# Performance work log

Hardware: AMD Instinct MI355X
Metric: run time of the kernel (lower is better)

## Reference

```python
import jax, jax.numpy as jnp
import numpy as np
from jax import lax

B, C_IN, T_FRAMES = 64, 128, 200
AUDIO_LEN = 48000
N_BANDS = 32


def _filter_shapes():
    lin = np.linspace(0.0, 1.0, N_BANDS, dtype=np.float32)
    fs = np.stack([
        np.exp(-0.5 * ((lin - 0.2) / 0.1) ** 2),
        np.exp(-0.5 * ((lin - 0.1) / 0.1) ** 2),
        np.exp(-0.5 * ((lin - 0.4) / 0.15) ** 2),
        np.exp(-0.5 * ((lin - 0.6) / 0.1) ** 2),
        np.linspace(0.1, 1.0, N_BANDS, dtype=np.float32) ** 2,
    ]).astype(np.float32)
    return fs


def _linear_interp(x, out_len):
    # PyTorch F.interpolate(mode='linear', align_corners=False) along last dim
    t_in = x.shape[-1]
    src = (jnp.arange(out_len, dtype=jnp.float32) + 0.5) * (t_in / out_len) - 0.5
    src = jnp.clip(src, 0.0, float(t_in - 1))
    i0 = jnp.floor(src).astype(jnp.int32)
    i1 = jnp.minimum(i0 + 1, t_in - 1)
    w = (src - i0).astype(x.dtype)
    return x[..., i0] * (1.0 - w) + x[..., i1] * w


def _conv1d(x, w, b, pad):
    y = lax.conv_general_dilated(x, w, (1,), [(pad, pad)],
                                 dimension_numbers=('NCH', 'OIH', 'NCH'))
    return y + b[None, :, None]


def _band_index(num_bins):
    # bin k belongs to band b iff int(b*num_bins/32) <= k < int((b+1)*num_bins/32)
    bounds = np.array([int(b * num_bins / N_BANDS) for b in range(N_BANDS + 1)])
    idx = np.searchsorted(bounds, np.arange(num_bins), side='right') - 1
    return np.clip(idx, 0, N_BANDS - 1)


def _forward(condition, f0, white_noise, w1, b1, w2, b2, w3, b3, w4, b4, audio_length):
    leaky = lambda v: jnp.where(v >= 0, v, 0.1 * v)
    is_voiced = (f0 > 0).astype(condition.dtype)[:, None, :]                 # [B,1,T]
    x = jnp.concatenate([condition, is_voiced], axis=1)                       # [B,129,T]
    h = leaky(_conv1d(x, w1, b1, 2))
    h = leaky(_conv1d(h, w2, b2, 1))
    h = leaky(_conv1d(h, w3, b3, 1))
    p = _conv1d(h, w4, b4, 0)                                                 # [B,40,T]
    inhal = jax.nn.sigmoid(p[:, 0:1])
    exhal = jax.nn.sigmoid(p[:, 1:2])
    pressure = jax.nn.sigmoid(p[:, 2:3])
    spectral_shape = jax.nn.softmax(p[:, 3:35], axis=1)                       # [B,32,T]
    turbulence = jax.nn.softmax(p[:, 35:40], axis=1)                          # [B,5,T]
    breath_features = jnp.concatenate([pressure, inhal, exhal], axis=1)       # [B,3,T]
    control = jnp.concatenate([inhal, exhal, pressure, turbulence], axis=1)   # [B,8,T]
    # --- FFT colored noise shaping (single block since L <= 60000) ---
    num_bins = audio_length // 2 + 1
    avg_shape = jnp.mean(spectral_shape, axis=2)                              # [B,32]
    gains = avg_shape[:, _band_index(num_bins)]                               # [B,bins]
    nfft = jnp.fft.rfft(white_noise[:, 0, :])                                 # [B,bins]
    shaped = jnp.fft.irfft(nfft * gains, n=audio_length)                      # [B,L]
    shaped = shaped / jnp.std(shaped, axis=1, ddof=1, keepdims=True) * 0.1
    breath_noise = shaped[:, None, :]                                         # [B,1,L]
    # --- linear upsample frame-rate controls to audio rate ---
    ctrl_a = _linear_interp(control, audio_length)                            # [B,8,L]
    voiced_a = _linear_interp(is_voiced, audio_length)                        # [B,1,L]
    inh_a, exh_a, pr_a = ctrl_a[:, 0:1], ctrl_a[:, 1:2], ctrl_a[:, 2:3]
    turb_a = ctrl_a[:, 3:8]                                                   # [B,5,L]
    breath = breath_noise * inh_a * (1.0 - voiced_a) + breath_noise * exh_a * pr_a
    # --- turbulence-location spectral filtering (vectorized over 5 locs) ---
    bfft = jnp.fft.rfft(breath[:, 0, :])                                      # [B,bins]
    fbins = _linear_interp(jnp.asarray(_filter_shapes())[None], num_bins)[0]  # [5,bins]
    loc_w = jnp.mean(turb_a, axis=2)                                          # [B,5]
    total_filter = loc_w @ fbins                                              # [B,bins]
    filtered = jnp.fft.irfft(bfft * total_filter, n=audio_length)[:, None, :]
    return filtered, breath_features


def setup_inputs() -> dict:
    key = jax.random.key(0)
    ks = jax.random.split(key, 7)
    s = 0.05
    return {
        'condition': jax.random.normal(ks[0], (B, C_IN, T_FRAMES), jnp.float32),
        'f0': jax.random.normal(ks[1], (B, T_FRAMES), jnp.float32),
        'white_noise': jax.random.normal(ks[2], (B, 1, AUDIO_LEN), jnp.float32),
        'w1': jax.random.normal(ks[3], (256, C_IN + 1, 5), jnp.float32) * s,
        'b1': jnp.zeros((256,), jnp.float32),
        'w2': jax.random.normal(ks[4], (128, 256, 3), jnp.float32) * s,
        'b2': jnp.zeros((128,), jnp.float32),
        'w3': jax.random.normal(ks[5], (64, 128, 3), jnp.float32) * s,
        'b3': jnp.zeros((64,), jnp.float32),
        'w4': jax.random.normal(ks[6], (40, 64, 1), jnp.float32) * s,
        'b4': jnp.zeros((40,), jnp.float32),
        'audio_length': AUDIO_LEN,
    }


def reference(condition, f0, white_noise, w1, b1, w2, b2, w3, b3, w4, b4, audio_length):
    return _forward(condition, f0, white_noise, w1, b1, w2, b2, w3, b3, w4, b4, audio_length)
```

## Files before the change

### kernel.cpp

```cpp
#include <hip/hip_runtime.h>
#include <math.h>

#define BB 64
#define T_FR 200
#define NA 48000
#define NBINS 24001

typedef __attribute__((ext_vector_type(4))) float f32x4;
typedef __attribute__((ext_vector_type(8))) short bf16x8;

__device__ __forceinline__ unsigned short f2bf(float x)
{
    unsigned u = __float_as_uint(x);
    u = (u + 0x7FFFu + ((u >> 16) & 1u)) >> 16;
    return (unsigned short)u;
}
__device__ __forceinline__ float bf2f(unsigned short h)
{
    return __uint_as_float(((unsigned)h) << 16);
}

__device__ __forceinline__ float2 cmul(float2 a, float2 b)
{
    return make_float2(a.x * b.x - a.y * b.y, a.x * b.y + a.y * b.x);
}
__device__ __forceinline__ float2 cadd(float2 a, float2 b){ return make_float2(a.x+b.x, a.y+b.y); }
__device__ __forceinline__ float2 csub(float2 a, float2 b){ return make_float2(a.x-b.x, a.y-b.y); }

__device__ __forceinline__ float2 cis_rev(float rev)
{
    return make_float2(__builtin_amdgcn_cosf(rev), __builtin_amdgcn_sinf(rev));
}

template<int R> __device__ __forceinline__ void fill_roots(float (&cr)[R], float (&si)[R]);
template<> __device__ __forceinline__ void fill_roots<3>(float (&cr)[3], float (&si)[3])
{
    const float S = 0.86602540378443865f;
    cr[0]=1.f; cr[1]=-0.5f; cr[2]=-0.5f;
    si[0]=0.f; si[1]=S;     si[2]=-S;
}
template<> __device__ __forceinline__ void fill_roots<5>(float (&cr)[5], float (&si)[5])
{
    cr[0]=1.f; cr[1]=0.30901699437494742f; cr[2]=-0.80901699437494742f;
    cr[3]=-0.80901699437494742f; cr[4]=0.30901699437494742f;
    si[0]=0.f; si[1]=0.95105651629515357f; si[2]=0.58778525229247313f;
    si[3]=-0.58778525229247313f; si[4]=-0.95105651629515357f;
}
template<> __device__ __forceinline__ void fill_roots<8>(float (&cr)[8], float (&si)[8])
{
    const float C = 0.70710678118654752f;
    cr[0]=1.f; cr[1]=C;  cr[2]=0.f;  cr[3]=-C; cr[4]=-1.f; cr[5]=-C;  cr[6]=0.f;  cr[7]=C;
    si[0]=0.f; si[1]=C;  si[2]=1.f;  si[3]=C;  si[4]=0.f;  si[5]=-C;  si[6]=-1.f; si[7]=-C;
}

template<int S, int R>
__device__ __forceinline__ void dftR(float2 (&v)[R])
{
    float cr[R], si[R];
    fill_roots<R>(cr, si);
    float2 o[R];
#pragma unroll
    for (int k = 0; k < R; ++k) {
        float re = 0.f, im = 0.f;
#pragma unroll
        for (int j = 0; j < R; ++j) {
            int m = (j * k) % R;
            float ur = cr[m], ui = (S > 0) ? si[m] : -si[m];
            re += v[j].x * ur - v[j].y * ui;
            im += v[j].x * ui + v[j].y * ur;
        }
        o[k] = make_float2(re, im);
    }
#pragma unroll
    for (int k = 0; k < R; ++k) v[k] = o[k];
}

__device__ __constant__ float C25R[17] = {1.f,0.968583161f,0.876306680f,0.728968627f,0.535826795f,0.309016994f,0.062790520f,-0.187381315f,-0.425779292f,-0.637423990f,-0.809016994f,-0.929776486f,-0.992114701f,-0.992114701f,-0.929776486f,-0.809016994f,-0.637423990f};
__device__ __constant__ float C25I[17] = {0.f,0.248689887f,0.481753674f,0.684547106f,0.844327926f,0.951056516f,0.998026728f,0.982287251f,0.904827052f,0.770513243f,0.587785252f,0.368124553f,0.125333234f,-0.125333234f,-0.368124553f,-0.587785252f,-0.770513243f};
__device__ __constant__ float C15R[9] = {1.f,0.913545458f,0.669130606f,0.309016994f,-0.104528463f,-0.5f,-0.809016994f,-0.978147601f,-0.978147601f};
__device__ __constant__ float C15I[9] = {0.f,0.406736643f,0.743144825f,0.951056516f,0.994521895f,0.866025404f,0.587785252f,0.207911691f,-0.207911691f};
__device__ __constant__ float C16R[10] = {1.f,0.923879533f,0.707106781f,0.382683432f,0.f,-0.382683432f,-0.707106781f,-0.923879533f,-1.f,-0.923879533f};
__device__ __constant__ float C16I[10] = {0.f,0.382683432f,0.707106781f,0.923879533f,1.f,0.923879533f,0.707106781f,0.382683432f,0.f,-0.382683432f};

template<int S> __device__ __forceinline__ float2 tw25(int m){ return make_float2(C25R[m], S>0? C25I[m] : -C25I[m]); }
template<int S> __device__ __forceinline__ float2 tw15(int m){ return make_float2(C15R[m], S>0? C15I[m] : -C15I[m]); }
template<int S> __device__ __forceinline__ float2 tw16(int m){ return make_float2(C16R[m], S>0? C16I[m] : -C16I[m]); }

template<int S> __device__ __forceinline__ void f4(float2& x0, float2& x1, float2& x2, float2& x3)
{
    float2 e = cadd(x0,x2), f = csub(x0,x2), g = cadd(x1,x3), h = csub(x1,x3);
    float2 r = (S<0) ? make_float2(h.y, -h.x) : make_float2(-h.y, h.x);
    x0 = cadd(e,g); x2 = csub(e,g); x1 = cadd(f,r); x3 = csub(f,r);
}

template<int S> __device__ __forceinline__ void fft16(float2 (&v)[16])
{
    float2 t[4][4];
#pragma unroll
    for (int q = 0; q < 4; ++q) {
        float2 a = v[q], b = v[4+q], c = v[8+q], d = v[12+q];
        f4<S>(a,b,c,d);
        t[q][0]=a; t[q][1]=b; t[q][2]=c; t[q][3]=d;
    }
#pragma unroll
    for (int q = 1; q < 4; ++q)
#pragma unroll
        for (int r = 1; r < 4; ++r)
            t[q][r] = cmul(t[q][r], tw16<S>(q*r));
#pragma unroll
    for (int r = 0; r < 4; ++r) {
        float2 a=t[0][r], b=t[1][r], c=t[2][r], d=t[3][r];
        f4<S>(a,b,c,d);
        v[r]=a; v[r+4]=b; v[r+8]=c; v[r+12]=d;
    }
}

template<int S> __device__ __forceinline__ void fft15(float2 (&v)[15])
{
    float2 t[5][3];
#pragma unroll
    for (int d = 0; d < 5; ++d) {
        float2 u[3] = { v[d], v[5+d], v[10+d] };
        dftR<S,3>(u);
        t[d][0]=u[0];
        t[d][1]=cmul(u[1], tw15<S>(d));
        t[d][2]=cmul(u[2], tw15<S>(2*d));
    }
#pragma unroll
    for (int e = 0; e < 3; ++e) {
        float2 u[5] = { t[0][e],t[1][e],t[2][e],t[3][e],t[4][e] };
        dftR<S,5>(u);
#pragma unroll
        for (int g = 0; g < 5; ++g) v[e + 3*g] = u[g];
    }
}

template<int S> __device__ __forceinline__ void fft25(float2 (&v)[25])
{
    float2 t[5][5];
#pragma unroll
    for (int d = 0; d < 5; ++d) {
        float2 u[5] = { v[d], v[5+d], v[10+d], v[15+d], v[20+d] };
        dftR<S,5>(u);
        t[d][0] = u[0];
#pragma unroll
        for (int e = 1; e < 5; ++e) t[d][e] = cmul(u[e], tw25<S>(d*e));
    }
#pragma unroll
    for (int e = 0; e < 5; ++e) {
        float2 u[5] = { t[0][e],t[1][e],t[2][e],t[3][e],t[4][e] };
        dftR<S,5>(u);
#pragma unroll
        for (int g = 0; g < 5; ++g) v[e + 5*g] = u[g];
    }
}

__device__ __forceinline__ int slotn(int f) { return 25 * (f & 7) + (f >> 3); }

__device__ __forceinline__ void pair_combine(float2 Za, float2 Zb, float g1, float g2,
                                             float2& C, float2& Cp, float& e1, float& e2)
{
    float2 X1 = make_float2(0.5f * (Za.x + Zb.x), 0.5f * (Za.y - Zb.y));
    float2 w  = make_float2(0.5f * (Za.x - Zb.x), 0.5f * (Za.y + Zb.y));
    float2 X2 = make_float2(w.y, -w.x);
    float2 Z1 = make_float2(g1 * X1.x, g1 * X1.y);
    float2 Z2 = make_float2(g2 * X2.x, g2 * X2.y);
    e1 = Z1.x * Z1.x + Z1.y * Z1.y;
    e2 = Z2.x * Z2.x + Z2.y * Z2.y;
    C  = make_float2(Z1.x - Z2.y,  Z1.y + Z2.x);
    Cp = make_float2(Z1.x + Z2.y, -Z1.y + Z2.x);
}

template<int NT, int TAPS, int CHUNKS, int CINP, int COUTP>
__global__ __launch_bounds__(256) void conv_mfma_kernel(
    const unsigned short* __restrict__ xT, int tRowsIn,
    const unsigned short* __restrict__ wT,
    const float* __restrict__ bias,
    unsigned short* __restrict__ outT, int tRowsOut, int tOffOut)
{
    const int b = blockIdx.y;
    const int t0 = blockIdx.x * 16;
    const int tid = threadIdx.x;
    const int wave = tid >> 6;
    const int lane = tid & 63;
    const int m = lane & 15;
    const int quad = lane >> 4;
    const int n0 = wave * (NT * 16);

    f32x4 acc[NT];
#pragma unroll
    for (int nt = 0; nt < NT; ++nt) acc[nt] = (f32x4){0.f, 0.f, 0.f, 0.f};

    const unsigned short* xb = xT + (size_t)b * tRowsIn * CINP;
#pragma unroll
    for (int kw = 0; kw < TAPS; ++kw) {
        const unsigned short* wk = wT + (size_t)kw * COUTP * CINP;
        const unsigned short* xrow = xb + (size_t)(t0 + kw + m) * CINP + quad * 8;
#pragma unroll
        for (int ch = 0; ch < CHUNKS; ++ch) {
            const int k0 = ch * 32;
            bf16x8 a = *(const bf16x8*)(xrow + k0);
#pragma unroll
            for (int nt = 0; nt < NT; ++nt) {
                bf16x8 bfr = *(const bf16x8*)(wk + (size_t)(n0 + nt * 16 + m) * CINP + k0 + quad * 8);
                acc[nt] = __builtin_amdgcn_mfma_f32_16x16x32_bf16(a, bfr, acc[nt], 0, 0, 0);
            }
        }
    }
#pragma unroll
    for (int nt = 0; nt < NT; ++nt) {
        const int n = n0 + nt * 16 + m;
        const float bz = bias[n];
#pragma unroll
        for (int r = 0; r < 4; ++r) {
            const int t = t0 + quad * 4 + r;
            if (t < 200) {
                float v = acc[nt][r] + bz;
                v = (v >= 0.f) ? v : 0.1f * v;
                outT[((size_t)b * tRowsOut + t + tOffOut) * COUTP + n] = f2bf(v);
            }
        }
    }
}

__global__ void prep_x1_kernel(const float* __restrict__ cond, const float* __restrict__ f0,
                               unsigned short* __restrict__ xpT1)
{
    int idx = blockIdx.x * 256 + threadIdx.x;
    const int total = BB * 212 * 160;
    if (idx >= total) return;
    int i = idx % 160;
    int rest = idx / 160;
    int tp = rest % 212;
    int b = rest / 212;
    int tt = tp - 2;
    float v = 0.f;
    if (tt >= 0 && tt < 200) {
        if (i < 128) v = cond[((size_t)b * 128 + i) * 200 + tt];
        else if (i == 128) v = (f0[b * 200 + tt] > 0.f) ? 1.f : 0.f;
    }
    xpT1[idx] = f2bf(v);
}

template<int TAPS, int CINR, int CINP, int COUTP>
__global__ void prep_w_kernel(const float* __restrict__ w, unsigned short* __restrict__ wT)
{
    int idx = blockIdx.x * 256 + threadIdx.x;
    const int total = TAPS * COUTP * CINP;
    if (idx >= total) return;
    int i = idx % CINP;
    int rest = idx / CINP;
    int o = rest % COUTP;
    int kw = rest / COUTP;
    float v = (i < CINR) ? w[((size_t)o * CINR + i) * TAPS + kw] : 0.f;
    wT[idx] = f2bf(v);
}

__global__ void zero16_kernel(uint4* __restrict__ p, int n16)
{
    int idx = blockIdx.x * 256 + threadIdx.x;
    if (idx < n16) p[idx] = make_uint4(0, 0, 0, 0);
}


__global__ __launch_bounds__(128) void passA_kernel(const float* __restrict__ wn,
                                                    float2* __restrict__ I)
{
    __shared__ float2 L[8 * 241];
    int q = blockIdx.y;
    const float* w1p = wn + (size_t)(2 * q) * NA;
    const float* w2p = wn + (size_t)(2 * q + 1) * NA;
    int n20 = blockIdx.x * 8;
    int tid = threadIdx.x;

    if (tid < 120) {
        int b = tid >> 3, j = tid & 7;
        int n2 = n20 + j;
        float2 v[16];
#pragma unroll
        for (int a = 0; a < 16; ++a) {
            int n = (15 * a + b) * 200 + n2;
            v[a] = make_float2(w1p[n], w2p[n]);
        }
        fft16<-1>(v);
#pragma unroll
        for (int f1 = 1; f1 < 16; ++f1)
            v[f1] = cmul(v[f1], cis_rev(-(float)(b * f1) * (1.f / 240.f)));
        float2* col = L + j * 241;
#pragma unroll
        for (int f1 = 0; f1 < 16; ++f1) col[f1 * 15 + b] = v[f1];
    }
    __syncthreads();
    {
        int f1 = tid >> 3, j = tid & 7;
        int n2 = n20 + j;
        float2* col = L + j * 241;
        float2 u[15];
#pragma unroll
        for (int b = 0; b < 15; ++b) u[b] = col[f1 * 15 + b];
        fft15<-1>(u);
#pragma unroll
        for (int f2 = 0; f2 < 15; ++f2) {
            int f = f1 + 16 * f2;
            I[(size_t)q * NA + (size_t)f * 200 + n2] =
                cmul(u[f2], cis_rev(-(float)(n2 * f) * (1.f / (float)NA)));
        }
    }
}

template<int MODE>
__global__ __launch_bounds__(256) void passB_kernel(float2* __restrict__ I,
    const float* __restrict__ avg_shape, const float* __restrict__ fbins,
    const float* __restrict__ loc_w, float* __restrict__ acc, float* __restrict__ z0)
{
    __shared__ float2 L[12 * 202];
    __shared__ float g1sh[32], g2sh[32];
    int q = blockIdx.y;
    int b1 = 2 * q, b2 = 2 * q + 1;
    int bx = blockIdx.x;
    int tid = threadIdx.x;
    if (MODE == 0) {
        if (tid < 32) { g1sh[tid] = avg_shape[b1 * 32 + tid]; g2sh[tid] = avg_shape[b2 * 32 + tid]; }
    } else {
        if (tid < 5) { g1sh[tid] = loc_w[b1 * 5 + tid]; g2sh[tid] = loc_w[b2 * 5 + tid]; }
    }
    int Rrow[12];
#pragma unroll
    for (int s = 0; s < 12; ++s) {
        int p = s >> 1;
        int pi = 6 * bx + p;
        Rrow[s] = (pi == 0) ? ((s & 1) ? 120 : 0) : ((s & 1) ? 240 - pi : pi);
    }
    for (int idx = tid; idx < 300; idx += 256) {
        int s = idx / 25, b = idx - 25 * s;
        const float2* g = I + (size_t)q * NA + (size_t)Rrow[s] * 200;
        float2 v[8];
#pragma unroll
        for (int a = 0; a < 8; ++a) v[a] = g[25 * a + b];
        dftR<-1, 8>(v);
#pragma unroll
        for (int f1 = 1; f1 < 8; ++f1)
            v[f1] = cmul(v[f1], cis_rev(-(float)(b * f1) * (1.f / 200.f)));
        float2* row = L + s * 202;
#pragma unroll
        for (int f1 = 0; f1 < 8; ++f1) row[f1 * 25 + b] = v[f1];
    }
    __syncthreads();
    if (tid < 96) {
        int s = tid >> 3, f1 = tid & 7;
        float2* row = L + s * 202;
        float2 u[25];
#pragma unroll
        for (int b = 0; b < 25; ++b) u[b] = row[f1 * 25 + b];
        fft25<-1>(u);
#pragma unroll
        for (int f2 = 0; f2 < 25; ++f2) row[f1 * 25 + f2] = u[f2];
    }
    __syncthreads();
    float part1 = 0.f, part2 = 0.f;
    for (int idx = tid; idx < 1206; idx += 256) {
        int p = idx / 201, t = idx - p * 201;
        int pi = 6 * bx + p;
        float2* rwA = L + (2 * p) * 202;
        float2* rwB = L + (2 * p + 1) * 202;
        int k = -1;
        float2 Za, Zb;
        int sa = 0, sb = 0;
        float2* wa = rwA; float2* wb = rwB;
        bool self1 = false;
        if (pi != 0) {
            if (t >= 200) continue;
            sa = slotn(t); sb = slotn(199 - t);
            Za = rwA[sa]; Zb = rwB[sb];
            k = pi + 240 * t;
        } else if (t < 101) {
            wa = rwA; wb = rwA;
            if (t == 0 || t == 100) {
                sa = slotn(t); sb = sa;
                Za = rwA[sa]; Zb = Za;
                k = 240 * t;
                self1 = true;
            } else {
                sa = slotn(t); sb = slotn(200 - t);
                Za = rwA[sa]; Zb = rwA[sb];
                k = 240 * t;
            }
        } else {
            int t2 = t - 101;
            if (t2 >= 100) continue;
            wa = rwB; wb = rwB;
            sa = slotn(t2); sb = slotn(199 - t2);
            Za = rwB[sa]; Zb = rwB[sb];
            k = 120 + 240 * t2;
        }
        int kbin = min(k, NA - k);
        float g1, g2;
        if (MODE == 0) {
            int jj = (kbin * 32) / NBINS;
            if (jj < 31 && (NBINS * (jj + 1)) / 32 <= kbin) ++jj;
            g1 = g1sh[jj]; g2 = g2sh[jj];
        } else {
            g1 = 0.f; g2 = 0.f;
#pragma unroll
            for (int c = 0; c < 5; ++c) {
                float fb = fbins[c * NBINS + kbin];
                g1 += g1sh[c] * fb; g2 += g2sh[c] * fb;
            }
        }
        float2 C, Cp; float e1, e2;
        pair_combine(Za, Zb, g1, g2, C, Cp, e1, e2);
        if (MODE == 0) {
            float wgt = self1 ? 1.f : 2.f;
            part1 += wgt * e1; part2 += wgt * e2;
            if (k == 0) { z0[b1] = g1 * Za.x; z0[b2] = g2 * Za.y; }
        }
        wa[sa] = make_float2(C.x * (1.f / NA), C.y * (1.f / NA));
        if (!self1) wb[sb] = make_float2(Cp.x * (1.f / NA), Cp.y * (1.f / NA));
    }
    if (MODE == 0) {
        for (int o = 32; o > 0; o >>= 1) {
            part1 += __shfl_down(part1, o);
            part2 += __shfl_down(part2, o);
        }
        if ((tid & 63) == 0) { atomicAdd(&acc[b1], part1); atomicAdd(&acc[b2], part2); }
    }
    __syncthreads();
    if (tid < 96) {
        int s = tid >> 3, f1 = tid & 7;
        float2* row = L + s * 202;
        float2 u[25];
#pragma unroll
        for (int f2 = 0; f2 < 25; ++f2) u[f2] = row[f1 * 25 + f2];
        fft25<+1>(u);
#pragma unroll
        for (int b = 0; b < 25; ++b) row[f1 * 25 + b] = u[b];
    }
    __syncthreads();
    for (int idx = tid; idx < 300; idx += 256) {
        int s = idx / 25, b = idx - 25 * s;
        float2* row = L + s * 202;
        float2 w[8];
#pragma unroll
        for (int f1 = 0; f1 < 8; ++f1) w[f1] = row[f1 * 25 + b];
#pragma unroll
        for (int f1 = 1; f1 < 8; ++f1)
            w[f1] = cmul(w[f1], cis_rev((float)(b * f1) * (1.f / 200.f)));
        dftR<+1, 8>(w);
        int rg = Rrow[s];
        float2* g = I + (size_t)q * NA + (size_t)rg * 200;
#pragma unroll
        for (int a = 0; a < 8; ++a) {
            int e = 25 * a + b;
            g[e] = cmul(w[a], cis_rev((float)(e * rg) * (1.f / (float)NA)));
        }
    }
}

__global__ __launch_bounds__(128) void passC_kernel(float2* __restrict__ I,
    const float* __restrict__ control, const float* __restrict__ f0,
    const float* __restrict__ scale)
{
    __shared__ float2 L[8 * 241];
    __shared__ float ctlA[600], ctlB[600];
    __shared__ float f0A[200], f0B[200];
    int q = blockIdx.y;
    int b1 = 2 * q, b2 = 2 * q + 1;
    int n20 = blockIdx.x * 8;
    int tid = threadIdx.x;
    for (int i = tid; i < 600; i += 128) {
        ctlA[i] = control[(size_t)b1 * 1600 + i];
        ctlB[i] = control[(size_t)b2 * 1600 + i];
    }
    for (int i = tid; i < 200; i += 128) {
        f0A[i] = f0[b1 * 200 + i];
        f0B[i] = f0[b2 * 200 + i];
    }
    {
        int f1 = tid >> 3, j = tid & 7;
        int n2 = n20 + j;
        float2 u[15];
#pragma unroll
        for (int f2 = 0; f2 < 15; ++f2)
            u[f2] = I[(size_t)q * NA + (size_t)(f1 + 16 * f2) * 200 + n2];
        fft15<+1>(u);
        float2* col = L + j * 241;
#pragma unroll
        for (int b = 0; b < 15; ++b) col[f1 * 15 + b] = u[b];
    }
    __syncthreads();
    if (tid < 120) {
        int b = tid >> 3, j = tid & 7;
        int n2 = n20 + j;
        float2* col = L + j * 241;
        float sc1 = scale[b1], sc2 = scale[b2];
        float2 w[16];
#pragma unroll
        for (int f1 = 0; f1 < 16; ++f1) w[f1] = col[f1 * 15 + b];
#pragma unroll
        for (int f1 = 1; f1 < 16; ++f1)
            w[f1] = cmul(w[f1], cis_rev((float)(b * f1) * (1.f / 240.f)));
        fft16<+1>(w);
#pragma unroll
        for (int a = 0; a < 16; ++a) {
            int n = 200 * (15 * a + b) + n2;
            float sf = ((float)n + 0.5f) * (1.f / 240.f) - 0.5f;
            sf = fminf(fmaxf(sf, 0.f), 199.f);
            int i0 = (int)sf;
            int i1 = min(i0 + 1, 199);
            float wt = sf - (float)i0, w0 = 1.f - wt;
            float inh = ctlA[i0] * w0 + ctlA[i1] * wt;
            float exh = ctlA[200 + i0] * w0 + ctlA[200 + i1] * wt;
            float pr  = ctlA[400 + i0] * w0 + ctlA[400 + i1] * wt;
            float vv  = (f0A[i0] > 0.f ? 1.f : 0.f) * w0 + (f0A[i1] > 0.f ? 1.f : 0.f) * wt;
            float m1 = inh * (1.f - vv) + exh * pr;
            inh = ctlB[i0] * w0 + ctlB[i1] * wt;
            exh = ctlB[200 + i0] * w0 + ctlB[200 + i1] * wt;
            pr  = ctlB[400 + i0] * w0 + ctlB[400 + i1] * wt;
            vv  = (f0B[i0] > 0.f ? 1.f : 0.f) * w0 + (f0B[i1] > 0.f ? 1.f : 0.f) * wt;
            float m2 = inh * (1.f - vv) + exh * pr;
            w[a] = make_float2(w[a].x * sc1 * m1, w[a].y * sc2 * m2);
        }
        fft16<-1>(w);
#pragma unroll
        for (int f1 = 1; f1 < 16; ++f1)
            w[f1] = cmul(w[f1], cis_rev(-(float)(b * f1) * (1.f / 240.f)));
#pragma unroll
        for (int f1 = 0; f1 < 16; ++f1) col[f1 * 15 + b] = w[f1];
    }
    __syncthreads();
    {
        int f1 = tid >> 3, j = tid & 7;
        int n2 = n20 + j;
        float2* col = L + j * 241;
        float2 u[15];
#pragma unroll
        for (int b = 0; b < 15; ++b) u[b] = col[f1 * 15 + b];
        fft15<-1>(u);
#pragma unroll
        for (int f2 = 0; f2 < 15; ++f2) {
            int f = f1 + 16 * f2;
            I[(size_t)q * NA + (size_t)f * 200 + n2] =
                cmul(u[f2], cis_rev(-(float)(n2 * f) * (1.f / (float)NA)));
        }
    }
}

__global__ __launch_bounds__(128) void passD_kernel(const float2* __restrict__ I,
                                                    float* __restrict__ out)
{
    __shared__ float2 L[8 * 241];
    int q = blockIdx.y;
    int b1 = 2 * q, b2 = 2 * q + 1;
    int n20 = blockIdx.x * 8;
    int tid = threadIdx.x;
    {
        int f1 = tid >> 3, j = tid & 7;
        int n2 = n20 + j;
        float2 u[15];
#pragma unroll
        for (int f2 = 0; f2 < 15; ++f2)
            u[f2] = I[(size_t)q * NA + (size_t)(f1 + 16 * f2) * 200 + n2];
        fft15<+1>(u);
        float2* col = L + j * 241;
#pragma unroll
        for (int b = 0; b < 15; ++b) col[f1 * 15 + b] = u[b];
    }
    __syncthreads();
    if (tid < 120) {
        int b = tid >> 3, j = tid & 7;
        int n2 = n20 + j;
        float2* col = L + j * 241;
        float2 w[16];
#pragma unroll
        for (int f1 = 0; f1 < 16; ++f1) w[f1] = col[f1 * 15 + b];
#pragma unroll
        for (int f1 = 1; f1 < 16; ++f1)
            w[f1] = cmul(w[f1], cis_rev((float)(b * f1) * (1.f / 240.f)));
        fft16<+1>(w);
#pragma unroll
        for (int a = 0; a < 16; ++a) {
            int n = 200 * (15 * a + b) + n2;
            out[(size_t)b1 * NA + n] = w[a].x;
            out[(size_t)b2 * NA + n] = w[a].y;
        }
    }
}

__global__ void init_kernel(float* __restrict__ acc, float* __restrict__ z0)
{
    int i = threadIdx.x;
    if (i < 64) { acc[i] = 0.f; z0[i] = 0.f; }
}

__global__ void finalize_scale(const float* __restrict__ acc, const float* __restrict__ z0,
                               float* __restrict__ scale)
{
    int b = threadIdx.x;
    if (b < 64) {
        float var = (acc[b] - z0[b] * z0[b]) / (48000.f * 47999.f);
        scale[b] = 0.1f / sqrtf(var);
    }
}

__global__ void head_kernel(const unsigned short* __restrict__ h3T, const float* __restrict__ w4,
                            const float* __restrict__ b4, float* __restrict__ control,
                            float* __restrict__ avg_shape, float* __restrict__ out_bf)
{
    __shared__ float w4s[40 * 64];
    __shared__ float b4s[40];
    __shared__ float sp[200 * 33];
    int b = blockIdx.x;
    for (int j = threadIdx.x; j < 40 * 64; j += 256) w4s[j] = w4[j];
    if (threadIdx.x < 40) b4s[threadIdx.x] = b4[threadIdx.x];
    __syncthreads();
    int t = threadIdx.x;
    if (t < 200) {
        float p[40];
#pragma unroll
        for (int o = 0; o < 40; ++o) p[o] = b4s[o];
        const unsigned short* hb = h3T + ((size_t)b * 200 + t) * 64;
        for (int i = 0; i < 64; ++i) {
            float h = bf2f(hb[i]);
#pragma unroll
            for (int o = 0; o < 40; ++o) p[o] += h * w4s[o * 64 + i];
        }
        float inh = 1.f / (1.f + expf(-p[0]));
        float exh = 1.f / (1.f + expf(-p[1]));
        float pr  = 1.f / (1.f + expf(-p[2]));
        float mx = p[3];
#pragma unroll
        for (int c = 1; c < 32; ++c) mx = fmaxf(mx, p[3 + c]);
        float e[32];
        float sum = 0.f;
#pragma unroll
        for (int c = 0; c < 32; ++c) { e[c] = expf(p[3 + c] - mx); sum += e[c]; }
        float inv = 1.f / sum;
#pragma unroll
        for (int c = 0; c < 32; ++c) sp[t * 33 + c] = e[c] * inv;
        float mx2 = p[35];
#pragma unroll
        for (int c = 1; c < 5; ++c) mx2 = fmaxf(mx2, p[35 + c]);
        float e2[5];
        float s2 = 0.f;
#pragma unroll
        for (int c = 0; c < 5; ++c) { e2[c] = expf(p[35 + c] - mx2); s2 += e2[c]; }
        float inv2 = 1.f / s2;
        float* ctl = control + (size_t)b * 8 * 200;
        ctl[0 * 200 + t] = inh;
        ctl[1 * 200 + t] = exh;
        ctl[2 * 200 + t] = pr;
#pragma unroll
        for (int c = 0; c < 5; ++c) ctl[(3 + c) * 200 + t] = e2[c] * inv2;
        float* bf = out_bf + (size_t)b * 3 * 200;
        bf[0 * 200 + t] = pr;
        bf[1 * 200 + t] = inh;
        bf[2 * 200 + t] = exh;
    }
    __syncthreads();
    if (t < 32) {
        float s = 0.f;
        for (int j = 0; j < 200; ++j) s += sp[j * 33 + t];
        avg_shape[b * 32 + t] = s * (1.f / 200.f);
    }
}

__global__ void locw_mean_kernel(const float* __restrict__ control, float* __restrict__ loc_w)
{
    int c = blockIdx.x, b = blockIdx.y;
    int tid = threadIdx.x;
    const float* src = control + ((size_t)b * 8 + 3 + c) * 200;
    float s = (tid < 200) ? src[tid] : 0.f;
    for (int o = 32; o > 0; o >>= 1) s += __shfl_down(s, o);
    __shared__ float red[4];
    if ((tid & 63) == 0) red[tid >> 6] = s;
    __syncthreads();
    if (tid == 0) loc_w[b * 5 + c] = (red[0] + red[1] + red[2] + red[3]) * (1.f / 200.f);
}

__device__ inline float filter_shape_val(int c, int i)
{
    float lin = (float)i * (1.f / 31.f);
    if (c == 0) { float z = (lin - 0.2f) * 10.f;          return expf(-0.5f * z * z); }
    if (c == 1) { float z = (lin - 0.1f) * 10.f;          return expf(-0.5f * z * z); }
    if (c == 2) { float z = (lin - 0.4f) * (1.f / 0.15f); return expf(-0.5f * z * z); }
    if (c == 3) { float z = (lin - 0.6f) * 10.f;          return expf(-0.5f * z * z); }
    float v = 0.1f + 0.9f * lin;
    return v * v;
}

__global__ void fbins_kernel(float* __restrict__ fbins)
{
    int k = blockIdx.x * 256 + threadIdx.x;
    if (k >= NBINS) return;
    float sf = (k + 0.5f) * (32.0f / 24001.0f) - 0.5f;
    sf = fminf(fmaxf(sf, 0.f), 31.f);
    int i0 = (int)sf;
    int i1 = min(i0 + 1, 31);
    float w = sf - (float)i0;
#pragma unroll
    for (int c = 0; c < 5; ++c)
        fbins[c * NBINS + k] = filter_shape_val(c, i0) * (1.f - w) + filter_shape_val(c, i1) * w;
}

extern "C" void kernel_launch(void* const* d_in, const int* in_sizes, int n_in,
                              void* d_out, int out_size, void* d_ws, size_t ws_size,
                              hipStream_t stream)
{
    const float* cond = (const float*)d_in[0];
    const float* f0   = (const float*)d_in[1];
    const float* wn   = (const float*)d_in[2];
    const float* w1   = (const float*)d_in[3];
    const float* b1   = (const float*)d_in[4];
    const float* w2   = (const float*)d_in[5];
    const float* b2   = (const float*)d_in[6];
    const float* w3   = (const float*)d_in[7];
    const float* b3   = (const float*)d_in[8];
    const float* w4   = (const float*)d_in[9];
    const float* b4   = (const float*)d_in[10];

    float* out = (float*)d_out;
    float* filtered = out;
    float* bf_out   = out + (size_t)BB * NA;

    char* ws = (char*)d_ws;
    size_t off = 0;
    float2* I = (float2*)(ws + off);            off += 24576000;
    unsigned short* xpT1 = (unsigned short*)(ws + off); off += (size_t)BB * 212 * 160 * 2;
    unsigned short* xpT2 = (unsigned short*)(ws + off); off += (size_t)BB * 210 * 256 * 2;
    unsigned short* xpT3 = (unsigned short*)(ws + off); off += (size_t)BB * 210 * 128 * 2;
    unsigned short* xpT4 = (unsigned short*)(ws + off); off += (size_t)BB * 200 * 64 * 2;
    unsigned short* wT1  = (unsigned short*)(ws + off); off += (size_t)5 * 256 * 160 * 2;
    unsigned short* wT2  = (unsigned short*)(ws + off); off += (size_t)3 * 128 * 256 * 2;
    unsigned short* wT3  = (unsigned short*)(ws + off); off += (size_t)3 * 64 * 128 * 2;
    float* control   = (float*)(ws + off);
    float* avg_shape = control + 102400;
    float* loc_w     = avg_shape + 2048;
    float* acc       = loc_w + 320;
    float* z0        = acc + 64;
    float* scale     = z0 + 64;
    float* fbins     = scale + 64;

    dim3 blk(256);

    init_kernel<<<1, 64, 0, stream>>>(acc, z0);

    {
        int n1 = BB * 212 * 160;
        prep_x1_kernel<<<dim3((n1 + 255) / 256), blk, 0, stream>>>(cond, f0, xpT1);
        int z2 = (BB * 210 * 256 * 2) / 16;
        zero16_kernel<<<dim3((z2 + 255) / 256), blk, 0, stream>>>((uint4*)xpT2, z2);
        int z3 = (BB * 210 * 128 * 2) / 16;
        zero16_kernel<<<dim3((z3 + 255) / 256), blk, 0, stream>>>((uint4*)xpT3, z3);
        prep_w_kernel<5, 129, 160, 256><<<dim3((5 * 256 * 160 + 255) / 256), blk, 0, stream>>>(w1, wT1);
        prep_w_kernel<3, 256, 256, 128><<<dim3((3 * 128 * 256 + 255) / 256), blk, 0, stream>>>(w2, wT2);
        prep_w_kernel<3, 128, 128, 64><<<dim3((3 * 64 * 128 + 255) / 256), blk, 0, stream>>>(w3, wT3);
    }

    conv_mfma_kernel<4, 5, 5, 160, 256><<<dim3(13, BB), blk, 0, stream>>>(
        xpT1, 212, wT1, b1, xpT2, 210, 1);
    conv_mfma_kernel<2, 3, 8, 256, 128><<<dim3(13, BB), blk, 0, stream>>>(
        xpT2, 210, wT2, b2, xpT3, 210, 1);
    conv_mfma_kernel<1, 3, 4, 128, 64><<<dim3(13, BB), blk, 0, stream>>>(
        xpT3, 210, wT3, b3, xpT4, 200, 0);

    head_kernel<<<dim3(BB), blk, 0, stream>>>(xpT4, w4, b4, control, avg_shape, bf_out);
    locw_mean_kernel<<<dim3(5, BB), blk, 0, stream>>>(control, loc_w);
    fbins_kernel<<<dim3((NBINS + 255) / 256), blk, 0, stream>>>(fbins);

    passA_kernel<<<dim3(25, 32), dim3(128), 0, stream>>>(wn, I);
    passB_kernel<0><<<dim3(20, 32), blk, 0, stream>>>(I, avg_shape, fbins, loc_w, acc, z0);
    finalize_scale<<<1, 64, 0, stream>>>(acc, z0, scale);
    passC_kernel<<<dim3(25, 32), dim3(128), 0, stream>>>(I, control, f0, scale);
    passB_kernel<1><<<dim3(20, 32), blk, 0, stream>>>(I, avg_shape, fbins, loc_w, acc, z0);
    passD_kernel<<<dim3(25, 32), dim3(128), 0, stream>>>(I, filtered);
}
```

Before: 367.6 us.

## Fuse forward fft25, spectral combine and inverse fft25 in registers per thread

For non-DC row pairs, each thread now loads one A row and its mirrored B row, runs the forward 25-point FFT, applies the filter/energy combine on the paired bins, and runs the inverse FFT, all in registers. This removes two shared-memory round trips and two barriers-worth of separate phases for most blocks. The special pi==0 pair keeps the old path, but only in block 0. The cost is more registers per thread (two 25-element complex arrays) and work spread over only 12 lanes per wave.

New measurement: 634.7 us. 1.73x slower.

```diff
diff --git a/kernel.cpp b/kernel.cpp
--- a/kernel.cpp
+++ b/kernel.cpp
@@ -169,6 +169,37 @@
     e2 = Z2.x * Z2.x + Z2.y * Z2.y;
     C  = make_float2(Z1.x - Z2.y,  Z1.y + Z2.x);
     Cp = make_float2(Z1.x + Z2.y, -Z1.y + Z2.x);
+}
+
+template<int MODE>
+__device__ __forceinline__ void comb_one(float2& A, float2& B, int k, float wgt, bool self1,
+                                         const float* __restrict__ g1sh, const float* __restrict__ g2sh,
+                                         const float* __restrict__ fbins,
+                                         float& part1, float& part2,
+                                         float* __restrict__ z0, int b1, int b2)
+{
+    int kbin = min(k, NA - k);
+    float g1, g2;
+    if (MODE == 0) {
+        int jj = (kbin * 32) / NBINS;
+        if (jj < 31 && (NBINS * (jj + 1)) / 32 <= kbin) ++jj;
+        g1 = g1sh[jj]; g2 = g2sh[jj];
+    } else {
+        g1 = 0.f; g2 = 0.f;
+#pragma unroll
+        for (int c = 0; c < 5; ++c) {
+            float fb = fbins[c * NBINS + kbin];
+            g1 += g1sh[c] * fb; g2 += g2sh[c] * fb;
+        }
+    }
+    float2 C, Cp; float e1, e2;
+    pair_combine(A, B, g1, g2, C, Cp, e1, e2);
+    if (MODE == 0) {
+        part1 += wgt * e1; part2 += wgt * e2;
+        if (k == 0) { z0[b1] = g1 * A.x; z0[b2] = g2 * A.y; }
+    }
+    A = make_float2(C.x * (1.f / NA), C.y * (1.f / NA));
+    if (!self1) B = make_float2(Cp.x * (1.f / NA), Cp.y * (1.f / NA));
 }
 
 template<int NT, int TAPS, int CHUNKS, int CINP, int COUTP>
@@ -346,76 +377,100 @@
         for (int f1 = 0; f1 < 8; ++f1) row[f1 * 25 + b] = v[f1];
     }
     __syncthreads();
-    if (tid < 96) {
-        int s = tid >> 3, f1 = tid & 7;
-        float2* row = L + s * 202;
-        float2 u[25];
-#pragma unroll
-        for (int b = 0; b < 25; ++b) u[b] = row[f1 * 25 + b];
-        fft25<-1>(u);
-#pragma unroll
-        for (int f2 = 0; f2 < 25; ++f2) row[f1 * 25 + f2] = u[f2];
-    }
-    __syncthreads();
     float part1 = 0.f, part2 = 0.f;
-    for (int idx = tid; idx < 1206; idx += 256) {
-        int p = idx / 201, t = idx - p * 201;
-        int pi = 6 * bx + p;
-        float2* rwA = L + (2 * p) * 202;
-        float2* rwB = L + (2 * p + 1) * 202;
-        int k = -1;
-        float2 Za, Zb;
-        int sa = 0, sb = 0;
-        float2* wa = rwA; float2* wb = rwB;
-        bool self1 = false;
-        if (pi != 0) {
-            if (t >= 200) continue;
-            sa = slotn(t); sb = slotn(199 - t);
-            Za = rwA[sa]; Zb = rwB[sb];
-            k = pi + 240 * t;
-        } else if (t < 101) {
-            wa = rwA; wb = rwA;
-            if (t == 0 || t == 100) {
-                sa = slotn(t); sb = sa;
-                Za = rwA[sa]; Zb = Za;
-                k = 240 * t;
-                self1 = true;
+    {
+        int lane = tid & 63;
+        int task = (tid >> 6) * 12 + lane;
+        if (lane < 12 && !(bx == 0 && (task >> 3) == 0)) {
+            int p = task >> 3, f1 = task & 7;
+            int pi = 6 * bx + p;
+            float2* rowA = L + (2 * p) * 202;
+            float2* rowB = L + (2 * p + 1) * 202;
+            float2 vA[25], vB[25];
+#pragma unroll
+            for (int b = 0; b < 25; ++b) vA[b] = rowA[f1 * 25 + b];
+            fft25<-1>(vA);
+#pragma unroll
+            for (int b = 0; b < 25; ++b) vB[b] = rowB[(7 - f1) * 25 + b];
+            fft25<-1>(vB);
+#pragma unroll
+            for (int f2 = 0; f2 < 25; ++f2) {
+                int k = pi + 240 * (f1 + 8 * f2);
+                comb_one<MODE>(vA[f2], vB[24 - f2], k, 2.f, false,
+                               g1sh, g2sh, fbins, part1, part2, z0, b1, b2);
+            }
+            fft25<+1>(vA);
+            fft25<+1>(vB);
+#pragma unroll
+            for (int b = 0; b < 25; ++b) rowA[f1 * 25 + b] = vA[b];
+#pragma unroll
+            for (int b = 0; b < 25; ++b) rowB[(7 - f1) * 25 + b] = vB[b];
+        }
+        if (bx == 0 && tid < 8) {
+#pragma unroll
+            for (int s = 0; s < 2; ++s) {
+                float2* row = L + s * 202;
+                float2 u[25];
+#pragma unroll
+                for (int b = 0; b < 25; ++b) u[b] = row[tid * 25 + b];
+                fft25<-1>(u);
+#pragma unroll
+                for (int f2 = 0; f2 < 25; ++f2) row[tid * 25 + f2] = u[f2];
+            }
+        }
+    }
+    __syncthreads();
+    if (bx == 0) {
+        float2* rwA = L;
+        float2* rwB = L + 202;
+        for (int t = tid; t < 201; t += 256) {
+            int sa, sb, k;
+            bool self1 = false;
+            float2 *wa, *wb;
+            float2 Za, Zb;
+            if (t < 101) {
+                wa = rwA; wb = rwA;
+                if (t == 0 || t == 100) {
+                    sa = slotn(t); sb = sa;
+                    Za = rwA[sa]; Zb = Za;
+                    k = 240 * t;
+                    self1 = true;
+                } else {
+                    sa = slotn(t); sb = slotn(200 - t);
+                    Za = rwA[sa]; Zb = rwA[sb];
+                    k = 240 * t;
+                }
             } else {
-                sa = slotn(t); sb = slotn(200 - t);
-                Za = rwA[sa]; Zb = rwA[sb];
-                k = 240 * t;
+                int t2 = t - 101;
+                wa = rwB; wb = rwB;
+                sa = slotn(t2); sb = slotn(199 - t2);
+                Za = rwB[sa]; Zb = rwB[sb];
+                k = 120 + 240 * t2;
             }
-        } else {
-            int t2 = t - 101;
-            if (t2 >= 100) continue;
-            wa = rwB; wb = rwB;
-            sa = slotn(t2); sb = slotn(199 - t2);
-            Za = rwB[sa]; Zb = rwB[sb];
-            k = 120 + 240 * t2;
-        }
-        int kbin = min(k, NA - k);
-        float g1, g2;
-        if (MODE == 0) {
-            int jj = (kbin * 32) / NBINS;
-            if (jj < 31 && (NBINS * (jj + 1)) / 32 <= kbin) ++jj;
-            g1 = g1sh[jj]; g2 = g2sh[jj];
-        } else {
-            g1 = 0.f; g2 = 0.f;
-#pragma unroll
-            for (int c = 0; c < 5; ++c) {
-                float fb = fbins[c * NBINS + kbin];
-                g1 += g1sh[c] * fb; g2 += g2sh[c] * fb;
+            int kbin = min(k, NA - k);
+            float g1, g2;
+            if (MODE == 0) {
+                int jj = (kbin * 32) / NBINS;
+                if (jj < 31 && (NBINS * (jj + 1)) / 32 <= kbin) ++jj;
+                g1 = g1sh[jj]; g2 = g2sh[jj];
+            } else {
+                g1 = 0.f; g2 = 0.f;
+#pragma unroll
+                for (int c = 0; c < 5; ++c) {
+                    float fb = fbins[c * NBINS + kbin];
+                    g1 += g1sh[c] * fb; g2 += g2sh[c] * fb;
+                }
             }
-        }
-        float2 C, Cp; float e1, e2;
-        pair_combine(Za, Zb, g1, g2, C, Cp, e1, e2);
-        if (MODE == 0) {
-            float wgt = self1 ? 1.f : 2.f;
-            part1 += wgt * e1; part2 += wgt * e2;
-            if (k == 0) { z0[b1] = g1 * Za.x; z0[b2] = g2 * Za.y; }
-        }
-        wa[sa] = make_float2(C.x * (1.f / NA), C.y * (1.f / NA));
-        if (!self1) wb[sb] = make_float2(Cp.x * (1.f / NA), Cp.y * (1.f / NA));
+            float2 C, Cp; float e1, e2;
+            pair_combine(Za, Zb, g1, g2, C, Cp, e1, e2);
+            if (MODE == 0) {
+                float wgt = self1 ? 1.f : 2.f;
+                part1 += wgt * e1; part2 += wgt * e2;
+                if (k == 0) { z0[b1] = g1 * Za.x; z0[b2] = g2 * Za.y; }
+            }
+            wa[sa] = make_float2(C.x * (1.f / NA), C.y * (1.f / NA));
+            if (!self1) wb[sb] = make_float2(Cp.x * (1.f / NA), Cp.y * (1.f / NA));
+        }
     }
     if (MODE == 0) {
         for (int o = 32; o > 0; o >>= 1) {
@@ -425,15 +480,17 @@
         if ((tid & 63) == 0) { atomicAdd(&acc[b1], part1); atomicAdd(&acc[b2], part2); }
     }
     __syncthreads();
-    if (tid < 96) {
-        int s = tid >> 3, f1 = tid & 7;
-        float2* row = L + s * 202;
-        float2 u[25];
-#pragma unroll
-        for (int f2 = 0; f2 < 25; ++f2) u[f2] = row[f1 * 25 + f2];
-        fft25<+1>(u);
-#pragma unroll
-        for (int b = 0; b < 25; ++b) row[f1 * 25 + b] = u[b];
+    if (bx == 0 && tid < 8) {
+#pragma unroll
+        for (int s = 0; s < 2; ++s) {
+            float2* row = L + s * 202;
+            float2 u[25];
+#pragma unroll
+            for (int f2 = 0; f2 < 25; ++f2) u[f2] = row[tid * 25 + f2];
+            fft25<+1>(u);
+#pragma unroll
+            for (int b = 0; b < 25; ++b) row[tid * 25 + b] = u[b];
+        }
     }
     __syncthreads();
     for (int idx = tid; idx < 300; idx += 256) {
```
